# Performance work log

Hardware: AMD Instinct MI355X
Metric: run time of the kernel (lower is better)

Reference implementation:

```python
import jax, jax.numpy as jnp
import numpy as np

LMAX, MMAX = 6, 2
M_SIZE = (7, 6, 5)
SPHERE_C, HID = 128, 128
N_NODES, N_EDGES = 5000, 20000
N_COEFF_FULL = (LMAX + 1) ** 2                       # 49, l-primary node coeffs
N_COEFF_M = M_SIZE[0] + 2 * (M_SIZE[1] + M_SIZE[2])  # 29, m-primary edge coeffs
EXTRA_M0 = LMAX * HID                                # gate scalars from conv1


def _gate_idx():
    # maps each gated m-primary coefficient (all but l=0,m=0) to its degree index l-1
    idx = [l - 1 for l in range(1, LMAX + 1)]            # m=0 block (l=1..lmax)
    for m in range(1, MMAX + 1):
        for _ in range(2):                               # (-m, +m) components
            idx += [l - 1 for l in range(m, LMAX + 1)]
    return np.asarray(idx, dtype=np.int32)

GATE_IDX = jnp.asarray(_gate_idx())


def _layer_norm(h, s, b):
    mu = jnp.mean(h, axis=-1, keepdims=True)
    var = jnp.var(h, axis=-1, keepdims=True)
    return (h - mu) * jax.lax.rsqrt(var + 1e-5) * s + b


def _radial(e, w0, b0, s0, bb0, w1, b1, s1, bb1, w2, b2):
    h = jax.nn.silu(_layer_norm(e @ w0 + b0, s0, bb0))
    h = jax.nn.silu(_layer_norm(h @ w1 + b1, s1, bb1))
    return h @ w2 + b2


def _so2_conv(x, w_m0, b_m0, w_m1, w_m2, extra, x_rad=None):
    # x: [E, N_COEFF_M, C_in] in m-primary layout
    E = x.shape[0]
    w_m = (w_m1, w_m2)
    outs = []
    # m = 0: plain linear over flattened (l, channel)
    x0 = x[:, :M_SIZE[0]].reshape(E, -1)
    off_rad = 0
    if x_rad is not None:
        x0 = x0 * x_rad[:, :x0.shape[1]]
        off_rad = x0.shape[1]
    x0 = x0 @ w_m0 + b_m0
    x0_extra = None
    if extra:
        x0_extra, x0 = x0[:, :extra], x0[:, extra:]
    outs.append(x0.reshape(E, M_SIZE[0], -1))
    off = M_SIZE[0]
    # m > 0: complex-style SO(2) convolution per order m
    for m in range(1, MMAX + 1):
        sz = M_SIZE[m]
        xm = x[:, off:off + 2 * sz].reshape(E, 2, -1)    # [E, 2, sz*C_in]
        if x_rad is not None:
            d = xm.shape[2]
            xm = xm * x_rad[:, off_rad:off_rad + d][:, None, :]
            off_rad += d
        y = xm @ w_m[m - 1]                              # [E, 2, 2*sz*C_out]
        half = y.shape[2] // 2
        yr, yi = y[..., :half], y[..., half:]
        out_r = yr[:, 0] - yi[:, 1]
        out_i = yr[:, 1] + yi[:, 0]
        outs.append(jnp.stack((out_r, out_i), axis=1).reshape(E, 2 * sz, -1))
        off += 2 * sz
    out = jnp.concatenate(outs, axis=1)
    return (out, x0_extra) if extra else out


def _gate_act(gating, x):
    # gating: [E, LMAX*HID], x: [E, N_COEFF_M, HID]
    g = jax.nn.sigmoid(gating).reshape(-1, LMAX, HID)[:, GATE_IDX]  # [E, N_COEFF_M-1, HID]
    scalars = jax.nn.silu(x[:, :1])
    return jnp.concatenate((scalars, x[:, 1:] * g), axis=1)


def _edgewise(x, x_edge, edge_index, wig, wig_inv, env, params):
    (rw0, rb0, rs0, rbb0, rw1, rb1, rs1, rbb1, rw2, rb2,
     c1w0, c1b0, c1w1, c1w2, c2w0, c2b0, c2w1, c2w2) = params
    # gather source/target node features and concat channels -> [E, 49, 2C]
    msg = jnp.concatenate((x[edge_index[0]], x[edge_index[1]]), axis=2)
    # Wigner rotation + M mapping: l-primary (49) -> m-primary (29)
    msg = jnp.einsum('emj,ejc->emc', wig, msg)
    x_rad = _radial(x_edge, rw0, rb0, rs0, rbb0, rw1, rb1, rs1, rbb1, rw2, rb2)
    msg, gating = _so2_conv(msg, c1w0, c1b0, c1w1, c1w2, EXTRA_M0, x_rad)
    msg = _gate_act(gating, msg)
    msg = _so2_conv(msg, c2w0, c2b0, c2w1, c2w2, 0)
    msg = msg * env
    # inverse rotation: m-primary (29) -> l-primary (49)
    msg = jnp.einsum('ejm,emc->ejc', wig_inv, msg)
    return jax.ops.segment_sum(msg, edge_index[1], num_segments=x.shape[0])


def setup_inputs() -> dict:
    key = jax.random.key(0)
    ks = iter(jax.random.split(key, 40))
    def W(shape):
        return jax.random.normal(next(ks), shape, jnp.float32) / np.sqrt(shape[0])
    C_IN1 = 2 * SPHERE_C
    rad_out = C_IN1 * sum(M_SIZE)  # 4608
    inp = {}
    inp['x'] = jax.random.normal(next(ks), (N_NODES, N_COEFF_FULL, SPHERE_C), jnp.float32)
    inp['x_edge'] = jax.random.normal(next(ks), (N_EDGES, 128), jnp.float32)
    inp['edge_distance'] = jax.random.uniform(next(ks), (N_EDGES,), jnp.float32, 0.1, 6.0)
    inp['edge_index'] = jax.random.randint(next(ks), (2, N_EDGES), 0, N_NODES)
    inp['wigner_and_M_mapping'] = jax.random.normal(next(ks), (N_EDGES, N_COEFF_M, N_COEFF_FULL), jnp.float32) / np.sqrt(N_COEFF_FULL)
    inp['wigner_and_M_mapping_inv'] = jax.random.normal(next(ks), (N_EDGES, N_COEFF_FULL, N_COEFF_M), jnp.float32) / np.sqrt(N_COEFF_M)
    inp['edge_envelope'] = jax.random.uniform(next(ks), (N_EDGES, 1, 1), jnp.float32)
    inp['rad_w0'] = W((128, 256)); inp['rad_b0'] = jnp.zeros((256,), jnp.float32)
    inp['rad_ln0_s'] = jnp.ones((256,), jnp.float32); inp['rad_ln0_b'] = jnp.zeros((256,), jnp.float32)
    inp['rad_w1'] = W((256, 256)); inp['rad_b1'] = jnp.zeros((256,), jnp.float32)
    inp['rad_ln1_s'] = jnp.ones((256,), jnp.float32); inp['rad_ln1_b'] = jnp.zeros((256,), jnp.float32)
    inp['rad_w2'] = W((256, rad_out)); inp['rad_b2'] = jnp.zeros((rad_out,), jnp.float32)
    inp['c1_w_m0'] = W((M_SIZE[0] * C_IN1, M_SIZE[0] * HID + EXTRA_M0))
    inp['c1_b_m0'] = jnp.zeros((M_SIZE[0] * HID + EXTRA_M0,), jnp.float32)
    inp['c1_w_m1'] = W((M_SIZE[1] * C_IN1, 2 * M_SIZE[1] * HID))
    inp['c1_w_m2'] = W((M_SIZE[2] * C_IN1, 2 * M_SIZE[2] * HID))
    inp['c2_w_m0'] = W((M_SIZE[0] * HID, M_SIZE[0] * SPHERE_C))
    inp['c2_b_m0'] = jnp.zeros((M_SIZE[0] * SPHERE_C,), jnp.float32)
    inp['c2_w_m1'] = W((M_SIZE[1] * HID, 2 * M_SIZE[1] * SPHERE_C))
    inp['c2_w_m2'] = W((M_SIZE[2] * HID, 2 * M_SIZE[2] * SPHERE_C))
    return inp


def reference(x, x_edge, edge_distance, edge_index, wigner_and_M_mapping,
              wigner_and_M_mapping_inv, edge_envelope,
              rad_w0, rad_b0, rad_ln0_s, rad_ln0_b, rad_w1, rad_b1, rad_ln1_s, rad_ln1_b,
              rad_w2, rad_b2, c1_w_m0, c1_b_m0, c1_w_m1, c1_w_m2,
              c2_w_m0, c2_b_m0, c2_w_m1, c2_w_m2):
    # edge_distance is accepted (module signature) but unused in the original forward
    params = (rad_w0, rad_b0, rad_ln0_s, rad_ln0_b, rad_w1, rad_b1, rad_ln1_s, rad_ln1_b,
              rad_w2, rad_b2, c1_w_m0, c1_b_m0, c1_w_m1, c1_w_m2,
              c2_w_m0, c2_b_m0, c2_w_m1, c2_w_m2)
    return _edgewise(x, x_edge, edge_index, wigner_and_M_mapping,
                     wigner_and_M_mapping_inv, edge_envelope, params)
```

## Files before the change

### kernel.cpp

```cpp
#include <hip/hip_runtime.h>
#include <stdint.h>


#define E_NUM   20000
#define NN      5000

typedef uint16_t u16;
typedef __bf16  bf16x8 __attribute__((ext_vector_type(8)));
typedef float   f32x4  __attribute__((ext_vector_type(4)));
typedef uint16_t u16x8 __attribute__((ext_vector_type(8)));

__device__ __forceinline__ float bf2f(u16 h){
  uint32_t u = ((uint32_t)h) << 16;
  return __builtin_bit_cast(float, u);
}
__device__ __forceinline__ u16 f2bf(float f){
  uint32_t u = __builtin_bit_cast(uint32_t, f);
  u += 0x7fffu + ((u >> 16) & 1u);
  return (u16)(u >> 16);
}
__device__ __forceinline__ float sigm(float x){ return 1.f / (1.f + __expf(-x)); }

__device__ __forceinline__ void gload16(const void* g, void* l){
  __builtin_amdgcn_global_load_lds(
      (const __attribute__((address_space(1))) void*)g,
      (__attribute__((address_space(3))) void*)l, 16, 0, 0);
}

__global__ void k_hist(const int* __restrict__ eidx, int* __restrict__ cnt){
  int e = blockIdx.x * 256 + threadIdx.x;
  if (e < E_NUM) atomicAdd(&cnt[eidx[E_NUM + e]], 1);
}
__global__ __launch_bounds__(256) void k_scan(const int* __restrict__ cnt,
                                              int* __restrict__ off){
  __shared__ int part[256];
  int t = threadIdx.x;
  int s = 0;
  #pragma unroll
  for (int i = 0; i < 20; ++i){
    int idx = t * 20 + i;
    if (idx < NN) s += cnt[idx];
  }
  part[t] = s;
  __syncthreads();
  if (t == 0){
    int run = 0;
    for (int i = 0; i < 256; ++i){ int v = part[i]; part[i] = run; run += v; }
  }
  __syncthreads();
  int run = part[t];
  #pragma unroll
  for (int i = 0; i < 20; ++i){
    int idx = t * 20 + i;
    if (idx < NN){ off[idx] = run; run += cnt[idx]; }
  }
}
__global__ void k_scatter(const int* __restrict__ eidx, int* __restrict__ off,
                          int* __restrict__ perm){
  int e = blockIdx.x * 256 + threadIdx.x;
  if (e < E_NUM){
    int pos = atomicAdd(&off[eidx[E_NUM + e]], 1);
    perm[pos] = e;
  }
}

__global__ void k_transpose_w(const float* __restrict__ in, u16* __restrict__ out,
                              int K, int N){
  __shared__ float t[32][33];
  int nb = blockIdx.x * 32, kb = blockIdx.y * 32;
  int tx = threadIdx.x & 31, ty = threadIdx.x >> 5;
  for (int i = ty; i < 32; i += 8)
    t[i][tx] = in[(size_t)(kb + i) * N + (nb + tx)];
  __syncthreads();
  for (int i = ty; i < 32; i += 8)
    out[(size_t)(nb + i) * K + (kb + tx)] = f2bf(t[tx][i]);
}

__global__ __launch_bounds__(256) void k_xpose(const float* __restrict__ x,
                                               u16* __restrict__ xT){
  __shared__ float t[6272];
  int n = blockIdx.x, tid = threadIdx.x;
  const float* xp = x + (size_t)n * 6272;
  for (int i = tid; i < 6272; i += 256) t[i] = xp[i];
  __syncthreads();
  int c = tid >> 1;
  int kh = (tid & 1) * 32;
  u16* o = xT + (size_t)n * 8192 + c * 64 + kh;
  #pragma unroll
  for (int q = 0; q < 4; ++q){
    u16x8 h;
    #pragma unroll
    for (int i = 0; i < 8; ++i){
      int k = kh + q * 8 + i;
      h[i] = (k < 49) ? f2bf(t[k * 128 + c]) : (u16)0;
    }
    *(u16x8*)(o + q * 8) = h;
  }
}

__global__ void k_gather_xe(const float* __restrict__ x_edge,
                            const int* __restrict__ perm,
                            u16* __restrict__ xe, int e0){
  int el = blockIdx.x, c = threadIdx.x;
  int pe = perm[e0 + el];
  xe[(size_t)el * 128 + c] = f2bf(x_edge[(size_t)pe * 128 + c]);
}

__global__ __launch_bounds__(256) void k_gemm_bt(
    const u16* __restrict__ A, const u16* __restrict__ A2, int lda,
    const u16* __restrict__ B,
    const float* __restrict__ bias,
    float* __restrict__ Cf, u16* __restrict__ Cb, u16* __restrict__ Cb2,
    int ldc, int M, int N, int K, int myb)
{
  __shared__ u16 As[2][4096];
  __shared__ u16 Bs[2][4096];
  const int tid  = threadIdx.x;
  const int lane = tid & 63;
  const int wave = tid >> 6;
  const int wm = wave >> 1, wn = wave & 1;
  const int fr = lane & 15, fq = lane >> 4;
  const int bn = blockIdx.x;
  int bm = blockIdx.y;
  if (bm >= myb){ bm -= myb; A = A2; Cb = Cb2; }
  const int row0 = bm * 128;

  const int lr  = lane >> 2;
  const int lg  = lane & 3;
  const int rA0 = wave * 32 + lr;
  const int rA1 = rA0 + 16;
  const int g0  = lg ^ ((rA0 >> 1) & 3);
  const int g1  = lg ^ ((rA1 >> 1) & 3);
  int gra0 = row0 + rA0; if (gra0 > M - 1) gra0 = M - 1;
  int gra1 = row0 + rA1; if (gra1 > M - 1) gra1 = M - 1;
  const u16* aS0 = A + (size_t)gra0 * lda + g0 * 8;
  const u16* aS1 = A + (size_t)gra1 * lda + g1 * 8;
  const u16* bS0 = B + (size_t)(bn * 128 + rA0) * K + g0 * 8;
  const u16* bS1 = B + (size_t)(bn * 128 + rA1) * K + g1 * 8;
  const int dA0 = (wave * 32) * 32;
  const int dA1 = (wave * 32 + 16) * 32;

  int aoff[4], boff[4];
  #pragma unroll
  for (int mi = 0; mi < 4; ++mi){
    int r = wm * 64 + mi * 16 + fr;
    aoff[mi] = r * 32 + (fq ^ ((r >> 1) & 3)) * 8;
  }
  #pragma unroll
  for (int ni = 0; ni < 4; ++ni){
    int r = wn * 64 + ni * 16 + fr;
    boff[ni] = r * 32 + (fq ^ ((r >> 1) & 3)) * 8;
  }

  f32x4 acc[4][4];
  #pragma unroll
  for (int i = 0; i < 4; ++i)
    #pragma unroll
    for (int j = 0; j < 4; ++j) acc[i][j] = (f32x4){0.f, 0.f, 0.f, 0.f};

  auto stage = [&](int buf, int k0){
    gload16(aS0 + k0, &As[buf][dA0]);
    gload16(aS1 + k0, &As[buf][dA1]);
    gload16(bS0 + k0, &Bs[buf][dA0]);
    gload16(bS1 + k0, &Bs[buf][dA1]);
  };

  stage(0, 0);
  __syncthreads();
  int cur = 0;
  for (int k0 = 0; k0 < K; k0 += 32){
    if (k0 + 32 < K) stage(cur ^ 1, k0 + 32);
    bf16x8 af[4], bfv[4];
    #pragma unroll
    for (int mi = 0; mi < 4; ++mi)
      af[mi] = __builtin_bit_cast(bf16x8, *(const u16x8*)&As[cur][aoff[mi]]);
    #pragma unroll
    for (int ni = 0; ni < 4; ++ni)
      bfv[ni] = __builtin_bit_cast(bf16x8, *(const u16x8*)&Bs[cur][boff[ni]]);
    #pragma unroll
    for (int mi = 0; mi < 4; ++mi)
      #pragma unroll
      for (int ni = 0; ni < 4; ++ni)
        acc[mi][ni] = __builtin_amdgcn_mfma_f32_16x16x32_bf16(af[mi], bfv[ni], acc[mi][ni], 0, 0, 0);
    __syncthreads();
    cur ^= 1;
  }

  #pragma unroll
  for (int ni = 0; ni < 4; ++ni){
    int col = bn * 128 + wn * 64 + ni * 16 + fr;
    float bv = bias ? bias[col] : 0.f;
    #pragma unroll
    for (int mi = 0; mi < 4; ++mi){
      #pragma unroll
      for (int i = 0; i < 4; ++i){
        int row = row0 + wm * 64 + mi * 16 + fq * 4 + i;
        if (row < M){
          float v = acc[mi][ni][i] + bv;
          if (Cb) Cb[(size_t)row * ldc + col] = f2bf(v);
          else    Cf[(size_t)row * ldc + col] = v;
        }
      }
    }
  }
}

__global__ __launch_bounds__(256) void k_ln_silu(
    const float* __restrict__ in, const float* __restrict__ sc,
    const float* __restrict__ bb, u16* __restrict__ out)
{
  int e = blockIdx.x, t = threadIdx.x;
  float v = in[(size_t)e * 256 + t];
  float s1 = v, s2 = v * v;
  #pragma unroll
  for (int off = 32; off > 0; off >>= 1){
    s1 += __shfl_down(s1, off);
    s2 += __shfl_down(s2, off);
  }
  __shared__ float r1[4], r2[4];
  if ((t & 63) == 0){ r1[t >> 6] = s1; r2[t >> 6] = s2; }
  __syncthreads();
  float S1 = r1[0] + r1[1] + r1[2] + r1[3];
  float S2 = r2[0] + r2[1] + r2[2] + r2[3];
  float mu  = S1 * (1.f / 256.f);
  float var = S2 * (1.f / 256.f) - mu * mu;
  float nv = (v - mu) * rsqrtf(var + 1e-5f) * sc[t] + bb[t];
  out[(size_t)e * 256 + t] = f2bf(nv * sigm(nv));
}

__global__ __launch_bounds__(256) void k_wig_fwd(
    const u16* __restrict__ xT, const int* __restrict__ eidx,
    const float* __restrict__ wig, const u16* __restrict__ xrad,
    u16* __restrict__ msgS, const int* __restrict__ perm, int e0)
{
  __shared__ u16 WL[32 * 64];
  int el = blockIdx.x, tid = threadIdx.x;
  int eg = perm[e0 + el];
  int lane = tid & 63, w = tid >> 6;

  const float* wp = wig + (size_t)eg * 1421;
  for (int idx = tid; idx < 2048; idx += 256){
    int m = idx >> 6, k = idx & 63;
    float v = (m < 29 && k < 49) ? wp[m * 49 + k] : 0.f;
    WL[m * 64 + ((((k >> 3) ^ (m & 7))) << 3) + (k & 7)] = f2bf(v);
  }

  const int fr = lane & 15, fq = lane >> 4;
  const int colbase = w * 64;
  int node = eidx[((w >> 1) ? E_NUM : 0) + eg];
  const u16* xb = xT + (size_t)node * 8192;
  bf16x8 bfv[4][2];
  #pragma unroll
  for (int ct = 0; ct < 4; ++ct)
    #pragma unroll
    for (int ks = 0; ks < 2; ++ks){
      int cc = ((w & 1) * 64) + ct * 16 + fr;
      bfv[ct][ks] = __builtin_bit_cast(bf16x8,
          *(const u16x8*)(xb + cc * 64 + (ks * 4 + fq) * 8));
    }
  __syncthreads();

  bf16x8 af[2][2];
  #pragma unroll
  for (int mt = 0; mt < 2; ++mt)
    #pragma unroll
    for (int ks = 0; ks < 2; ++ks){
      int m = mt * 16 + fr;
      int g = ks * 4 + fq;
      af[mt][ks] = __builtin_bit_cast(bf16x8,
          *(const u16x8*)&WL[m * 64 + ((g ^ (m & 7)) << 3)]);
    }
  f32x4 acc[2][4];
  #pragma unroll
  for (int mt = 0; mt < 2; ++mt)
    #pragma unroll
    for (int ct = 0; ct < 4; ++ct) acc[mt][ct] = (f32x4){0.f,0.f,0.f,0.f};
  #pragma unroll
  for (int mt = 0; mt < 2; ++mt)
    #pragma unroll
    for (int ct = 0; ct < 4; ++ct)
      #pragma unroll
      for (int ks = 0; ks < 2; ++ks)
        acc[mt][ct] = __builtin_amdgcn_mfma_f32_16x16x32_bf16(
            af[mt][ks], bfv[ct][ks], acc[mt][ct], 0, 0, 0);

  const u16* xr = xrad + (size_t)el * 4608;
  u16* o = msgS + (size_t)el * 7424;
  #pragma unroll
  for (int mt = 0; mt < 2; ++mt)
    #pragma unroll
    for (int ct = 0; ct < 4; ++ct){
      int col = colbase + ct * 16 + fr;
      #pragma unroll
      for (int r = 0; r < 4; ++r){
        int m = mt * 16 + fq * 4 + r;
        if (m < 29){
          int rr = (m < 13) ? m : (m < 24 ? m - 6 : m - 11);
          o[m * 256 + col] = f2bf(acc[mt][ct][r] * bf2f(xr[rr * 256 + col]));
        }
      }
    }
}

__global__ __launch_bounds__(128) void k_gate(
    const u16* __restrict__ c1m0, const u16* __restrict__ y10, const u16* __restrict__ y11,
    const u16* __restrict__ y20, const u16* __restrict__ y21, u16* __restrict__ msg2)
{
  int e = blockIdx.x, c = threadIdx.x;
  __shared__ float g[768];
  const u16* gp = c1m0 + (size_t)e * 1664;
  for (int i = c; i < 768; i += 128) g[i] = sigm(bf2f(gp[i]));
  __syncthreads();
  const u16* x0 = gp + 768;
  u16* o = msg2 + (size_t)e * 3712;
  { float v = bf2f(x0[c]); o[c] = f2bf(v * sigm(v)); }
  #pragma unroll
  for (int r = 1; r < 7; ++r)
    o[r * 128 + c] = f2bf(bf2f(x0[r * 128 + c]) * g[(r - 1) * 128 + c]);
  const u16* a0 = y10 + (size_t)e * 1536;
  const u16* a1 = y11 + (size_t)e * 1536;
  #pragma unroll
  for (int k = 0; k < 6; ++k){
    float orr = bf2f(a0[k * 128 + c]) - bf2f(a1[768 + k * 128 + c]);
    float oii = bf2f(a1[k * 128 + c]) + bf2f(a0[768 + k * 128 + c]);
    float gv = g[k * 128 + c];
    o[(7 + k)  * 128 + c] = f2bf(orr * gv);
    o[(13 + k) * 128 + c] = f2bf(oii * gv);
  }
  const u16* b0 = y20 + (size_t)e * 1280;
  const u16* b1 = y21 + (size_t)e * 1280;
  #pragma unroll
  for (int k = 0; k < 5; ++k){
    float orr = bf2f(b0[k * 128 + c]) - bf2f(b1[640 + k * 128 + c]);
    float oii = bf2f(b1[k * 128 + c]) + bf2f(b0[640 + k * 128 + c]);
    float gv = g[(1 + k) * 128 + c];
    o[(19 + k) * 128 + c] = f2bf(orr * gv);
    o[(24 + k) * 128 + c] = f2bf(oii * gv);
  }
}

__global__ __launch_bounds__(128) void k_recomb2(
    const u16* __restrict__ m3x0, const u16* __restrict__ z10, const u16* __restrict__ z11,
    const u16* __restrict__ z20, const u16* __restrict__ z21, const float* __restrict__ env,
    u16* __restrict__ msg3T, const int* __restrict__ perm, int e0)
{
  int e = blockIdx.x, c = threadIdx.x;
  float ev = env[perm[e0 + e]];
  u16 v[32];
  const u16* x0 = m3x0 + (size_t)e * 896;
  #pragma unroll
  for (int r = 0; r < 7; ++r) v[r] = f2bf(bf2f(x0[r * 128 + c]) * ev);
  const u16* a0 = z10 + (size_t)e * 1536;
  const u16* a1 = z11 + (size_t)e * 1536;
  #pragma unroll
  for (int k = 0; k < 6; ++k){
    float orr = bf2f(a0[k * 128 + c]) - bf2f(a1[768 + k * 128 + c]);
    float oii = bf2f(a1[k * 128 + c]) + bf2f(a0[768 + k * 128 + c]);
    v[7 + k]  = f2bf(orr * ev);
    v[13 + k] = f2bf(oii * ev);
  }
  const u16* b0 = z20 + (size_t)e * 1280;
  const u16* b1 = z21 + (size_t)e * 1280;
  #pragma unroll
  for (int k = 0; k < 5; ++k){
    float orr = bf2f(b0[k * 128 + c]) - bf2f(b1[640 + k * 128 + c]);
    float oii = bf2f(b1[k * 128 + c]) + bf2f(b0[640 + k * 128 + c]);
    v[19 + k] = f2bf(orr * ev);
    v[24 + k] = f2bf(oii * ev);
  }
  v[29] = 0; v[30] = 0; v[31] = 0;
  u16* o = msg3T + (size_t)e * 4096 + c * 32;
  #pragma unroll
  for (int q = 0; q < 4; ++q)
    *(u16x8*)(o + q * 8) = *(const u16x8*)(&v[q * 8]);
}

__global__ __launch_bounds__(256) void k_wig_inv(
    const u16* __restrict__ msg3T, const float* __restrict__ winv,
    const int* __restrict__ eidx, float* __restrict__ out,
    const int* __restrict__ perm, int e0, int cm)
{
  __shared__ u16 WV[64 * 32];
  int el = blockIdx.x, tid = threadIdx.x;
  int i = e0 + el;
  int d = eidx[E_NUM + perm[i]];
  if (el > 0 && eidx[E_NUM + perm[i - 1]] == d) return;
  int lane = tid & 63, w = tid >> 6;
  const int fr = lane & 15, fq = lane >> 4;
  const int jr = w * 16 + fr;

  f32x4 acc[8];
  #pragma unroll
  for (int ct = 0; ct < 8; ++ct) acc[ct] = (f32x4){0.f,0.f,0.f,0.f};

  int tend = e0 + cm;
  for (int t = i; t < tend; ++t){
    int pe = perm[t];
    if (t > i && eidx[E_NUM + pe] != d) break;
    __syncthreads();
    const float* wp = winv + (size_t)pe * 1421;
    for (int idx = tid; idx < 2048; idx += 256){
      int j = idx >> 5, m = idx & 31;
      float v = (j < 49 && m < 29) ? wp[j * 29 + m] : 0.f;
      WV[j * 32 + (((m >> 3) ^ (j & 3)) << 3) + (m & 7)] = f2bf(v);
    }
    __syncthreads();
    bf16x8 a = __builtin_bit_cast(bf16x8,
        *(const u16x8*)&WV[jr * 32 + ((fq ^ (jr & 3)) << 3)]);
    const u16* bp = msg3T + (size_t)(t - e0) * 4096;
    #pragma unroll
    for (int ct = 0; ct < 8; ++ct){
      bf16x8 b = __builtin_bit_cast(bf16x8,
          *(const u16x8*)(bp + (ct * 16 + fr) * 32 + fq * 8));
      acc[ct] = __builtin_amdgcn_mfma_f32_16x16x32_bf16(a, b, acc[ct], 0, 0, 0);
    }
  }

  float* op = out + (size_t)d * 6272;
  #pragma unroll
  for (int ct = 0; ct < 8; ++ct){
    int c = ct * 16 + fr;
    #pragma unroll
    for (int r = 0; r < 4; ++r){
      int j = w * 16 + fq * 4 + r;
      if (j < 49) atomicAdd(op + j * 128 + c, acc[ct][r]);
    }
  }
}

extern "C" void kernel_launch(void* const* d_in, const int* in_sizes, int n_in,
                              void* d_out, int out_size, void* d_ws, size_t ws_size,
                              hipStream_t stream)
{
  (void)in_sizes; (void)n_in;
  const float* x       = (const float*)d_in[0];
  const float* x_edge  = (const float*)d_in[1];
  const int*   eidx    = (const int*)d_in[3];
  const float* wig     = (const float*)d_in[4];
  const float* wig_inv = (const float*)d_in[5];
  const float* env     = (const float*)d_in[6];
  const float* rad_w0  = (const float*)d_in[7];
  const float* rad_b0  = (const float*)d_in[8];
  const float* ln0_s   = (const float*)d_in[9];
  const float* ln0_b   = (const float*)d_in[10];
  const float* rad_w1  = (const float*)d_in[11];
  const float* rad_b1  = (const float*)d_in[12];
  const float* ln1_s   = (const float*)d_in[13];
  const float* ln1_b   = (const float*)d_in[14];
  const float* rad_w2  = (const float*)d_in[15];
  const float* rad_b2  = (const float*)d_in[16];
  const float* c1w0    = (const float*)d_in[17];
  const float* c1b0    = (const float*)d_in[18];
  const float* c1w1    = (const float*)d_in[19];
  const float* c1w2    = (const float*)d_in[20];
  const float* c2w0    = (const float*)d_in[21];
  const float* c2b0    = (const float*)d_in[22];
  const float* c2w1    = (const float*)d_in[23];
  const float* c2w2    = (const float*)d_in[24];
  float* out = (float*)d_out;

  char* base = (char*)d_ws;
  size_t off = 0;
  auto alloc = [&](size_t bytes) -> char* {
    off = (off + 255) & ~(size_t)255;
    char* r = base + off;
    off += bytes;
    return r;
  };

  u16* wtR0  = (u16*)alloc((size_t)256  * 128  * 2);
  u16* wtR1  = (u16*)alloc((size_t)256  * 256  * 2);
  u16* wtR2  = (u16*)alloc((size_t)4608 * 256  * 2);
  u16* wtC10 = (u16*)alloc((size_t)1664 * 1792 * 2);
  u16* wtC11 = (u16*)alloc((size_t)1536 * 1536 * 2);
  u16* wtC12 = (u16*)alloc((size_t)1280 * 1280 * 2);
  u16* wtC20 = (u16*)alloc((size_t)896  * 896  * 2);
  u16* wtC21 = (u16*)alloc((size_t)1536 * 768  * 2);
  u16* wtC22 = (u16*)alloc((size_t)1280 * 640  * 2);
  u16* xT    = (u16*)alloc((size_t)NN * 8192 * 2);
  int* cnt   = (int*)alloc(NN * 4);
  int* soff  = (int*)alloc(NN * 4);
  int* perm  = (int*)alloc(E_NUM * 4);

  size_t fixed_end = (off + 65536) & ~(size_t)65535;
  size_t avail = (ws_size > fixed_end + (1u << 20)) ? (ws_size - fixed_end - (1u << 20)) : 0;
  long CH0 = (long)(avail / 40960);
  if (CH0 > E_NUM) CH0 = E_NUM;
  if (CH0 < 64) CH0 = 64;
  int nch = (int)((E_NUM + CH0 - 1) / CH0);
  int CH = (E_NUM + nch - 1) / nch;
  if (CH > CH0) CH = (int)CH0;

  off = fixed_end;
  const size_t C = (size_t)CH;
  u16*   xe   = (u16*)alloc(C * 128 * 2);
  float* tmp  = (float*)alloc(C * 256 * 4);
  u16*   h0   = (u16*)alloc(C * 256 * 2);
  u16*   h1   = (u16*)alloc(C * 256 * 2);
  u16* region1 = (u16*)alloc(C * 4608 * 2);
  u16* region2 = (u16*)alloc(C * 7424 * 2);
  u16* region3 = (u16*)alloc(C * 7296 * 2);
  u16* xrad = region1;
  u16* msg2 = region1;
  u16* msgS = region2;
  u16* m3x0 = region2;
  u16* z10  = region2 + C * 896;
  u16* z11  = region2 + C * 2432;
  u16* z20  = region2 + C * 3968;
  u16* z21  = region2 + C * 5248;
  u16* c1m0b = region3;
  u16* y10   = region3 + C * 1664;
  u16* y11   = region3 + C * 3200;
  u16* y20   = region3 + C * 4736;
  u16* y21   = region3 + C * 6016;
  u16* msg3T = region3;

  hipMemsetAsync(d_out, 0, (size_t)out_size * sizeof(float), stream);
  hipMemsetAsync(cnt, 0, NN * 4, stream);

  k_hist<<<(E_NUM + 255) / 256, 256, 0, stream>>>(eidx, cnt);
  k_scan<<<1, 256, 0, stream>>>(cnt, soff);
  k_scatter<<<(E_NUM + 255) / 256, 256, 0, stream>>>(eidx, soff, perm);
  k_xpose<<<NN, 256, 0, stream>>>(x, xT);

  auto tw = [&](const float* in, u16* o, int K, int N){
    k_transpose_w<<<dim3(N / 32, K / 32), 256, 0, stream>>>(in, o, K, N);
  };
  tw(rad_w0, wtR0, 128, 256);
  tw(rad_w1, wtR1, 256, 256);
  tw(rad_w2, wtR2, 256, 4608);
  tw(c1w0, wtC10, 1792, 1664);
  tw(c1w1, wtC11, 1536, 1536);
  tw(c1w2, wtC12, 1280, 1280);
  tw(c2w0, wtC20, 896, 896);
  tw(c2w1, wtC21, 768, 1536);
  tw(c2w2, wtC22, 640, 1280);

  auto gemm = [&](const u16* A, const u16* A2, int lda, const u16* B,
                  const float* bias, float* Cf, u16* Cb, u16* Cb2,
                  int ldc, int M, int N, int K){
    int myb = (M + 127) / 128;
    k_gemm_bt<<<dim3(N / 128, A2 ? 2 * myb : myb), 256, 0, stream>>>(
        A, A2, lda, B, bias, Cf, Cb, Cb2, ldc, M, N, K, myb);
  };

  for (int e0 = 0; e0 < E_NUM; e0 += CH){
    int cm = E_NUM - e0 < CH ? E_NUM - e0 : CH;

    k_gather_xe<<<cm, 128, 0, stream>>>(x_edge, perm, xe, e0);

    gemm(xe, nullptr, 128, wtR0, rad_b0, tmp, nullptr, nullptr, 256, cm, 256, 128);
    k_ln_silu<<<cm, 256, 0, stream>>>(tmp, ln0_s, ln0_b, h0);
    gemm(h0, nullptr, 256, wtR1, rad_b1, tmp, nullptr, nullptr, 256, cm, 256, 256);
    k_ln_silu<<<cm, 256, 0, stream>>>(tmp, ln1_s, ln1_b, h1);
    gemm(h1, nullptr, 256, wtR2, rad_b2, nullptr, xrad, nullptr, 4608, cm, 4608, 256);

    k_wig_fwd<<<cm, 256, 0, stream>>>(xT, eidx, wig, xrad, msgS, perm, e0);

    gemm(msgS,        nullptr,      7424, wtC10, c1b0,
         nullptr, c1m0b, nullptr, 1664, cm, 1664, 1792);
    gemm(msgS + 1792, msgS + 3328,  7424, wtC11, nullptr,
         nullptr, y10, y11, 1536, cm, 1536, 1536);
    gemm(msgS + 4864, msgS + 6144,  7424, wtC12, nullptr,
         nullptr, y20, y21, 1280, cm, 1280, 1280);

    k_gate<<<cm, 128, 0, stream>>>(c1m0b, y10, y11, y20, y21, msg2);

    gemm(msg2,        nullptr,      3712, wtC20, c2b0,
         nullptr, m3x0, nullptr, 896, cm, 896, 896);
    gemm(msg2 + 896,  msg2 + 1664,  3712, wtC21, nullptr,
         nullptr, z10, z11, 1536, cm, 1536, 768);
    gemm(msg2 + 2432, msg2 + 3072,  3712, wtC22, nullptr,
         nullptr, z20, z21, 1280, cm, 1280, 640);

    k_recomb2<<<cm, 128, 0, stream>>>(m3x0, z10, z11, z20, z21, env, msg3T, perm, e0);

    k_wig_inv<<<cm, 256, 0, stream>>>(msg3T, wig_inv, eidx, out, perm, e0, cm);
  }
}
```

Baseline: 2.521 ms.

## Fuse SO(2) conv GEMMs into one segmented grouped launch with XCD swizzle

Replaces three separate GEMM launches per SO(2) convolution with a single grouped kernel that dispatches five segments (m0, m1 real/imag, m2 real/imag) from one flat block index. Block IDs are remapped across the 8 XCDs so consecutive tiles of a segment share an XCD's L2. The aim is to cut launch overhead and the tail idle time of the smaller GEMMs by filling the GPU with one larger grid. The cost is a per-block segment lookup and a larger kernel argument struct.

```diff
diff --git a/kernel.cpp b/kernel.cpp
--- a/kernel.cpp
+++ b/kernel.cpp
@@ -25,6 +25,13 @@
   __builtin_amdgcn_global_load_lds(
       (const __attribute__((address_space(1))) void*)g,
       (__attribute__((address_space(3))) void*)l, 16, 0, 0);
+}
+
+__device__ __forceinline__ int swz8(int orig, int nwg){
+  int q = nwg >> 3, r = nwg & 7;
+  int x = orig & 7, p = orig >> 3;
+  int base = (x < r) ? x * (q + 1) : r * (q + 1) + (x - r) * q;
+  return base + p;
 }
 
 __global__ void k_hist(const int* __restrict__ eidx, int* __restrict__ cnt){
@@ -106,23 +113,23 @@
   xe[(size_t)el * 128 + c] = f2bf(x_edge[(size_t)pe * 128 + c]);
 }
 
-__global__ __launch_bounds__(256) void k_gemm_bt(
-    const u16* __restrict__ A, const u16* __restrict__ A2, int lda,
-    const u16* __restrict__ B,
-    const float* __restrict__ bias,
-    float* __restrict__ Cf, u16* __restrict__ Cb, u16* __restrict__ Cb2,
-    int ldc, int M, int N, int K, int myb)
-{
-  __shared__ u16 As[2][4096];
-  __shared__ u16 Bs[2][4096];
+struct Seg {
+  const u16* A; const u16* B; u16* C; const float* bias;
+  int M, N, K, lda, blk0;
+};
+struct Seg5 { Seg s[5]; int nwg; };
+
+__device__ __forceinline__ void gemm_tile(
+    const u16* __restrict__ A, int lda, const u16* __restrict__ B,
+    const float* __restrict__ bias, float* __restrict__ Cf,
+    u16* __restrict__ Cb, int ldc, int M, int N, int K,
+    int bm, int bn, u16* As , u16* Bs )
+{
   const int tid  = threadIdx.x;
   const int lane = tid & 63;
   const int wave = tid >> 6;
   const int wm = wave >> 1, wn = wave & 1;
   const int fr = lane & 15, fq = lane >> 4;
-  const int bn = blockIdx.x;
-  int bm = blockIdx.y;
-  if (bm >= myb){ bm -= myb; A = A2; Cb = Cb2; }
   const int row0 = bm * 128;
 
   const int lr  = lane >> 2;
@@ -159,10 +166,10 @@
     for (int j = 0; j < 4; ++j) acc[i][j] = (f32x4){0.f, 0.f, 0.f, 0.f};
 
   auto stage = [&](int buf, int k0){
-    gload16(aS0 + k0, &As[buf][dA0]);
-    gload16(aS1 + k0, &As[buf][dA1]);
-    gload16(bS0 + k0, &Bs[buf][dA0]);
-    gload16(bS1 + k0, &Bs[buf][dA1]);
+    gload16(aS0 + k0, &As[buf * 4096 + dA0]);
+    gload16(aS1 + k0, &As[buf * 4096 + dA1]);
+    gload16(bS0 + k0, &Bs[buf * 4096 + dA0]);
+    gload16(bS1 + k0, &Bs[buf * 4096 + dA1]);
   };
 
   stage(0, 0);
@@ -173,10 +180,10 @@
     bf16x8 af[4], bfv[4];
     #pragma unroll
     for (int mi = 0; mi < 4; ++mi)
-      af[mi] = __builtin_bit_cast(bf16x8, *(const u16x8*)&As[cur][aoff[mi]]);
+      af[mi] = __builtin_bit_cast(bf16x8, *(const u16x8*)&As[cur * 4096 + aoff[mi]]);
     #pragma unroll
     for (int ni = 0; ni < 4; ++ni)
-      bfv[ni] = __builtin_bit_cast(bf16x8, *(const u16x8*)&Bs[cur][boff[ni]]);
+      bfv[ni] = __builtin_bit_cast(bf16x8, *(const u16x8*)&Bs[cur * 4096 + boff[ni]]);
     #pragma unroll
     for (int mi = 0; mi < 4; ++mi)
       #pragma unroll
@@ -203,6 +210,35 @@
       }
     }
   }
+}
+
+__global__ __launch_bounds__(256) void k_gemm_bt(
+    const u16* __restrict__ A, int lda, const u16* __restrict__ B,
+    const float* __restrict__ bias, float* __restrict__ Cf,
+    u16* __restrict__ Cb, int ldc, int M, int N, int K)
+{
+  __shared__ u16 As[2 * 4096];
+  __shared__ u16 Bs[2 * 4096];
+  gemm_tile(A, lda, B, bias, Cf, Cb, ldc, M, N, K,
+            blockIdx.y, blockIdx.x, As, Bs);
+}
+
+__global__ __launch_bounds__(256) void k_gemm_seg(Seg5 g)
+{
+  __shared__ u16 As[2 * 4096];
+  __shared__ u16 Bs[2 * 4096];
+  int wgid = swz8(blockIdx.x, g.nwg);
+  Seg sg = g.s[4];
+  if (wgid < g.s[4].blk0) sg = g.s[3];
+  if (wgid < g.s[3].blk0) sg = g.s[2];
+  if (wgid < g.s[2].blk0) sg = g.s[1];
+  if (wgid < g.s[1].blk0) sg = g.s[0];
+  int local = wgid - sg.blk0;
+  int nbx = sg.N >> 7;
+  int bn = local % nbx;
+  int bm = local / nbx;
+  gemm_tile(sg.A, sg.lda, sg.B, sg.bias, nullptr, sg.C, sg.N,
+            sg.M, sg.N, sg.K, bm, bn, As, Bs);
 }
 
 __global__ __launch_bounds__(256) void k_ln_silu(
@@ -536,42 +572,63 @@
   tw(c2w1, wtC21, 768, 1536);
   tw(c2w2, wtC22, 640, 1280);
 
-  auto gemm = [&](const u16* A, const u16* A2, int lda, const u16* B,
-                  const float* bias, float* Cf, u16* Cb, u16* Cb2,
-                  int ldc, int M, int N, int K){
-    int myb = (M + 127) / 128;
-    k_gemm_bt<<<dim3(N / 128, A2 ? 2 * myb : myb), 256, 0, stream>>>(
-        A, A2, lda, B, bias, Cf, Cb, Cb2, ldc, M, N, K, myb);
+  auto gemm = [&](const u16* A, int lda, const u16* B, const float* bias,
+                  float* Cf, u16* Cb, int ldc, int M, int N, int K){
+    k_gemm_bt<<<dim3(N / 128, (M + 127) / 128), 256, 0, stream>>>(
+        A, lda, B, bias, Cf, Cb, ldc, M, N, K);
   };
 
   for (int e0 = 0; e0 < E_NUM; e0 += CH){
     int cm = E_NUM - e0 < CH ? E_NUM - e0 : CH;
+    int mb = (cm + 127) / 128;
 
     k_gather_xe<<<cm, 128, 0, stream>>>(x_edge, perm, xe, e0);
 
-    gemm(xe, nullptr, 128, wtR0, rad_b0, tmp, nullptr, nullptr, 256, cm, 256, 128);
+    gemm(xe, 128, wtR0, rad_b0, tmp, nullptr, 256, cm, 256, 128);
     k_ln_silu<<<cm, 256, 0, stream>>>(tmp, ln0_s, ln0_b, h0);
-    gemm(h0, nullptr, 256, wtR1, rad_b1, tmp, nullptr, nullptr, 256, cm, 256, 256);
+    gemm(h0, 256, wtR1, rad_b1, tmp, nullptr, 256, cm, 256, 256);
     k_ln_silu<<<cm, 256, 0, stream>>>(tmp, ln1_s, ln1_b, h1);
-    gemm(h1, nullptr, 256, wtR2, rad_b2, nullptr, xrad, nullptr, 4608, cm, 4608, 256);
+    gemm(h1, 256, wtR2, rad_b2, nullptr, xrad, 4608, cm, 4608, 256);
 
     k_wig_fwd<<<cm, 256, 0, stream>>>(xT, eidx, wig, xrad, msgS, perm, e0);
 
-    gemm(msgS,        nullptr,      7424, wtC10, c1b0,
-         nullptr, c1m0b, nullptr, 1664, cm, 1664, 1792);
-    gemm(msgS + 1792, msgS + 3328,  7424, wtC11, nullptr,
-         nullptr, y10, y11, 1536, cm, 1536, 1536);
-    gemm(msgS + 4864, msgS + 6144,  7424, wtC12, nullptr,
-         nullptr, y20, y21, 1280, cm, 1280, 1280);
+    {
+      Seg5 g;
+      int b = 0;
+      auto mk = [&](const u16* A, const u16* B, u16* Cb, const float* bias,
+                    int N, int K) -> Seg {
+        Seg s{A, B, Cb, bias, cm, N, K, 7424, b};
+        b += (N >> 7) * mb;
+        return s;
+      };
+      g.s[0] = mk(msgS,        wtC10, c1m0b, c1b0,   1664, 1792);
+      g.s[1] = mk(msgS + 1792, wtC11, y10,   nullptr, 1536, 1536);
+      g.s[2] = mk(msgS + 3328, wtC11, y11,   nullptr, 1536, 1536);
+      g.s[3] = mk(msgS + 4864, wtC12, y20,   nullptr, 1280, 1280);
+      g.s[4] = mk(msgS + 6144, wtC12, y21,   nullptr, 1280, 1280);
+      g.nwg = b;
+      k_gemm_seg<<<b, 256, 0, stream>>>(g);
+    }
 
     k_gate<<<cm, 128, 0, stream>>>(c1m0b, y10, y11, y20, y21, msg2);
 
-    gemm(msg2,        nullptr,      3712, wtC20, c2b0,
-         nullptr, m3x0, nullptr, 896, cm, 896, 896);
-    gemm(msg2 + 896,  msg2 + 1664,  3712, wtC21, nullptr,
-         nullptr, z10, z11, 1536, cm, 1536, 768);
-    gemm(msg2 + 2432, msg2 + 3072,  3712, wtC22, nullptr,
-         nullptr, z20, z21, 1280, cm, 1280, 640);
+    {
+      Seg5 g;
+      int b = 0;
+      auto mk = [&](const u16* A, const u16* B, u16* Cb, const float* bias,
+                    int N, int K) -> Seg {
+        Seg s{A, B, Cb, bias, cm, N, K, 3712, b};
+        b += (N >> 7) * mb;
+        return s;
+      };
+      g.s[0] = mk(msg2,        wtC20, m3x0, c2b0,   896,  896);
+      g.s[1] = mk(msg2 + 896,  wtC21, z10,  nullptr, 1536, 768);
+      g.s[2] = mk(msg2 + 1664, wtC21, z11,  nullptr, 1536, 768);
+      g.s[3] = mk(msg2 + 2432, wtC22, z20,  nullptr, 1280, 640);
+      g.s[4] = mk(msg2 + 3072, wtC22, z21,  nullptr, 1280, 640);
+      g.nwg = b;
+      k_gemm_seg<<<b, 256, 0, stream>>>(g);
+    }
 
     k_recomb2<<<cm, 128, 0, stream>>>(m3x0, z10, z11, z20, z21, env, msg3T, perm, e0);
 
```

After: 2.438 ms. -3.3%, faster.
